# Performance work log

Hardware: AMD Instinct MI355X
Metric: run time of the kernel (lower is better)

## Reference

```python
import jax, jax.numpy as jnp
import numpy as np

N = 25000
E = 400000
IN_DIM = 512
H = 8
D = 64
ALPHA = 0.2  # leaky relu negative slope


def setup_inputs() -> dict:
    key = jax.random.key(0)
    k1, k2, k3, k4, k5 = jax.random.split(key, 5)
    inputs = jax.random.normal(k1, (N, IN_DIM), dtype=jnp.float32)
    src = jax.random.randint(k2, (E,), 0, N)
    dst = jnp.arange(E) % N  # every node has E/N inbound edges -> normalizer > 0
    # parameters (xavier-normal-ish scale)
    W = jax.random.normal(k3, (H * D, IN_DIM), dtype=jnp.float32) * (1.414 * (2.0 / (IN_DIM + H * D)) ** 0.5)
    attn_l = jax.random.normal(k4, (H, D), dtype=jnp.float32) * (1.414 * (2.0 / (D + 1)) ** 0.5)
    attn_r = jax.random.normal(k5, (H, D), dtype=jnp.float32) * (1.414 * (2.0 / (D + 1)) ** 0.5)
    return {"inputs": inputs, "W": W, "attn_l": attn_l, "attn_r": attn_r, "src": src, "dst": dst}


def reference(inputs, W, attn_l, attn_r, src, dst):
    # node projection: [N, H, D]
    ft = (inputs @ W.T).reshape(N, H, D)
    # per-node attention scalars per head: [N, H]
    a1 = jnp.einsum('nhd,hd->nh', ft, attn_l)
    a2 = jnp.einsum('nhd,hd->nh', ft, attn_r)
    # edge scores with leaky relu: [E, H]
    e = a1[src] + a2[dst]
    e = jnp.where(e > 0, e, ALPHA * e)
    # numerically stable edge softmax over incoming edges of each dst node
    emax = jax.ops.segment_max(e, dst, num_segments=N)  # [N, H]
    scores = jnp.exp(e - emax[dst])                      # [E, H]
    z = jax.ops.segment_sum(scores, dst, num_segments=N)  # [N, H]
    # weighted scatter-sum aggregation: [N, H, D]
    msg = ft[src] * scores[:, :, None]                   # [E, H, D]
    agg = jax.ops.segment_sum(msg, dst, num_segments=N)
    return agg / z[:, :, None]
```

## Files before the change

### kernel.cpp

```cpp
#include <hip/hip_runtime.h>
#include <math.h>

#define N_NODES 25000
#define E_EDGES 400000
#define IN_DIM  512
#define H_HEADS 8
#define D_HEAD  64
#define OUT_DIM 512
#define ALPHA   0.2f
#define EPN     16

typedef __attribute__((ext_vector_type(8))) short short8;
typedef __attribute__((ext_vector_type(4))) float floatx4;

__device__ __forceinline__ unsigned short f2bf(float x) {
    unsigned u = __float_as_uint(x);
    u += 0x7fffu + ((u >> 16) & 1u);
    return (unsigned short)(u >> 16);
}

#define GBM 128
#define GBN 256
#define GBK 32
#define STR 40

__global__ __launch_bounds__(512) void gemm_bf(const float* __restrict__ A,
                                               const float* __restrict__ W,
                                               const float* __restrict__ attn_l,
                                               const float* __restrict__ attn_r,
                                               unsigned short* __restrict__ ftb,
                                               float* __restrict__ a1g,
                                               float* __restrict__ a2g) {
    __shared__ unsigned short As[GBM * STR];
    __shared__ unsigned short Bs[GBN * STR];

    const int t = threadIdx.x;
    const int mbase = blockIdx.x * GBM;
    const int nbase = blockIdx.y * GBN;

    const int arow = t >> 2;
    const int akoff = (t & 3) * 8;
    const int brow = t >> 1;
    const int bkoff = (t & 1) * 16;

    const int wave = t >> 6;
    const int wm = wave & 1;
    const int wn = wave >> 1;
    const int lane = t & 63;
    const int lr = lane & 15;
    const int lq = lane >> 4;

    floatx4 acc[4][4] = {};

    const unsigned short* a_rd = As + (wm * 64 + lr) * STR + lq * 8;
    const unsigned short* b_rd = Bs + (wn * 64 + lr) * STR + lq * 8;

    const int an = mbase + arow;
    const bool a_ok = (an < N_NODES);
    const float* a_ptr0 = A + (size_t)(a_ok ? an : 0) * IN_DIM + akoff;
    const float* b_ptr0 = W + (size_t)(nbase + brow) * IN_DIM + bkoff;
    unsigned short* a_wr = As + arow * STR + akoff;
    unsigned short* b_wr = Bs + brow * STR + bkoff;

    for (int k0 = 0; k0 < IN_DIM; k0 += GBK) {
        {
            const float4* p = (const float4*)(a_ptr0 + k0);
            float4 v0 = p[0], v1 = p[1];
            if (!a_ok) { v0 = v1 = make_float4(0.f, 0.f, 0.f, 0.f); }
            short8 s0;
            s0[0]=f2bf(v0.x); s0[1]=f2bf(v0.y); s0[2]=f2bf(v0.z); s0[3]=f2bf(v0.w);
            s0[4]=f2bf(v1.x); s0[5]=f2bf(v1.y); s0[6]=f2bf(v1.z); s0[7]=f2bf(v1.w);
            *(short8*)a_wr = s0;
        }
        {
            const float4* p = (const float4*)(b_ptr0 + k0);
            float4 v0 = p[0], v1 = p[1], v2 = p[2], v3 = p[3];
            short8 s0, s1;
            s0[0]=f2bf(v0.x); s0[1]=f2bf(v0.y); s0[2]=f2bf(v0.z); s0[3]=f2bf(v0.w);
            s0[4]=f2bf(v1.x); s0[5]=f2bf(v1.y); s0[6]=f2bf(v1.z); s0[7]=f2bf(v1.w);
            s1[0]=f2bf(v2.x); s1[1]=f2bf(v2.y); s1[2]=f2bf(v2.z); s1[3]=f2bf(v2.w);
            s1[4]=f2bf(v3.x); s1[5]=f2bf(v3.y); s1[6]=f2bf(v3.z); s1[7]=f2bf(v3.w);
            *(short8*)(b_wr + 0) = s0;
            *(short8*)(b_wr + 8) = s1;
        }
        __syncthreads();

        short8 af[4], bf[4];
        #pragma unroll
        for (int i = 0; i < 4; ++i) af[i] = *(const short8*)(a_rd + i * 16 * STR);
        #pragma unroll
        for (int j = 0; j < 4; ++j) bf[j] = *(const short8*)(b_rd + j * 16 * STR);
        #pragma unroll
        for (int i = 0; i < 4; ++i)
            #pragma unroll
            for (int j = 0; j < 4; ++j)
                acc[i][j] = __builtin_amdgcn_mfma_f32_16x16x32_bf16(af[i], bf[j], acc[i][j], 0, 0, 0);
        __syncthreads();
    }

    const int h = blockIdx.y * 4 + wn;
    float al[4], ar[4];
    #pragma unroll
    for (int j = 0; j < 4; ++j) {
        al[j] = attn_l[h * D_HEAD + j * 16 + lr];
        ar[j] = attn_r[h * D_HEAD + j * 16 + lr];
    }
    #pragma unroll
    for (int i = 0; i < 4; ++i) {
        #pragma unroll
        for (int r = 0; r < 4; ++r) {
            float s1 = 0.f, s2 = 0.f;
            #pragma unroll
            for (int j = 0; j < 4; ++j) {
                s1 += acc[i][j][r] * al[j];
                s2 += acc[i][j][r] * ar[j];
            }
            #pragma unroll
            for (int off = 1; off < 16; off <<= 1) {
                s1 += __shfl_xor(s1, off, 64);
                s2 += __shfl_xor(s2, off, 64);
            }
            if (lr == 0) {
                int n = mbase + wm * 64 + i * 16 + lq * 4 + r;
                if (n < N_NODES) {
                    a1g[n * H_HEADS + h] = s1;
                    a2g[n * H_HEADS + h] = s2;
                }
            }
        }
    }

    #pragma unroll
    for (int i = 0; i < 4; ++i) {
        #pragma unroll
        for (int j = 0; j < 4; ++j) {
            const int nrow = mbase + wm * 64 + i * 16 + lq * 4;
            const int col = nbase + wn * 64 + j * 16 + lr;
            #pragma unroll
            for (int r = 0; r < 4; ++r) {
                int nn = nrow + r;
                if (nn < N_NODES)
                    ftb[(size_t)nn * OUT_DIM + col] = f2bf(acc[i][j][r]);
            }
        }
    }
}

__global__ __launch_bounds__(256) void agg_kernel(const unsigned short* __restrict__ ftb,
                                                  const float* __restrict__ a1,
                                                  const float* __restrict__ a2,
                                                  const int* __restrict__ src,
                                                  float* __restrict__ out) {
    __shared__ int   s_src[4][EPN];
    __shared__ float s_w[4][H_HEADS][EPN];
    __shared__ float s_z[4][H_HEADS];

    const int t = threadIdx.x;
    const int nd = t >> 6;
    const int r  = t & 63;
    const int v  = blockIdx.x * 4 + nd;

    if (r < EPN) s_src[nd][r] = src[v + r * N_NODES];
    __syncthreads();

    {
        const int h  = r >> 3;
        const int jp = r & 7;
        const float a2v = a2[v * H_HEADS + h];
        int s0i = s_src[nd][jp * 2], s1i = s_src[nd][jp * 2 + 1];
        float x0 = a1[s0i * H_HEADS + h] + a2v;
        float x1 = a1[s1i * H_HEADS + h] + a2v;
        float e0 = x0 > 0.f ? x0 : ALPHA * x0;
        float e1 = x1 > 0.f ? x1 : ALPHA * x1;
        float m = fmaxf(e0, e1);
        #pragma unroll
        for (int off = 1; off < 8; off <<= 1) m = fmaxf(m, __shfl_xor(m, off, 64));
        float w0 = __expf(e0 - m), w1 = __expf(e1 - m);
        s_w[nd][h][jp * 2]     = w0;
        s_w[nd][h][jp * 2 + 1] = w1;
        float z = w0 + w1;
        #pragma unroll
        for (int off = 1; off < 8; off <<= 1) z += __shfl_xor(z, off, 64);
        if (jp == 0) s_z[nd][h] = z;
    }
    __syncthreads();

    const int h   = r >> 3;
    const int oct = r & 7;
    const size_t coff = (size_t)h * D_HEAD + oct * 8;

    float acc[8] = {};
    #pragma unroll
    for (int jj = 0; jj < EPN; ++jj) {
        float wj = s_w[nd][h][jj];
        const unsigned short* p = ftb + (size_t)s_src[nd][jj] * OUT_DIM + coff;
        uint4 q = *(const uint4*)p;
        acc[0] += wj * __uint_as_float(q.x << 16);
        acc[1] += wj * __uint_as_float(q.x & 0xffff0000u);
        acc[2] += wj * __uint_as_float(q.y << 16);
        acc[3] += wj * __uint_as_float(q.y & 0xffff0000u);
        acc[4] += wj * __uint_as_float(q.z << 16);
        acc[5] += wj * __uint_as_float(q.z & 0xffff0000u);
        acc[6] += wj * __uint_as_float(q.w << 16);
        acc[7] += wj * __uint_as_float(q.w & 0xffff0000u);
    }
    float iz = 1.f / s_z[nd][h];
    float* op = out + (size_t)v * OUT_DIM + coff;
    float4 o0 = make_float4(acc[0]*iz, acc[1]*iz, acc[2]*iz, acc[3]*iz);
    float4 o1 = make_float4(acc[4]*iz, acc[5]*iz, acc[6]*iz, acc[7]*iz);
    *(float4*)(op + 0) = o0;
    *(float4*)(op + 4) = o1;
}

extern "C" void kernel_launch(void* const* d_in, const int* in_sizes, int n_in,
                              void* d_out, int out_size, void* d_ws, size_t ws_size,
                              hipStream_t stream) {
    const float* inputs = (const float*)d_in[0];
    const float* W      = (const float*)d_in[1];
    const float* attn_l = (const float*)d_in[2];
    const float* attn_r = (const float*)d_in[3];
    const int*   src    = (const int*)d_in[4];

    float* out = (float*)d_out;
    unsigned short* ftb = (unsigned short*)d_ws;
    float* a1 = (float*)(ftb + (size_t)N_NODES * OUT_DIM);
    float* a2 = a1 + (size_t)N_NODES * H_HEADS;

    dim3 gemm_grid((N_NODES + GBM - 1) / GBM, OUT_DIM / GBN);
    gemm_bf<<<gemm_grid, 512, 0, stream>>>(inputs, W, attn_l, attn_r, ftb, a1, a2);

    agg_kernel<<<N_NODES / 4, 256, 0, stream>>>(ftb, a1, a2, src, out);
}
```

Baseline: 192.3 us.

## Pre-convert inputs to bf16 and stream GEMM tiles directly into LDS

A separate conversion kernel turns the inputs and W to bf16 once. The GEMM then loads tiles with global_load_lds straight into shared memory, and each block computes a full 64x512 output tile. That way each A row is read once rather than once per column block, and per-element conversion leaves the GEMM inner loop. The GEMM output overwrites the bf16 input buffer in place to save workspace. The risks are an extra memory pass, bank conflicts from the unpadded LDS layout, and the last block reading rows past N.

```diff
diff --git a/kernel.cpp b/kernel.cpp
--- a/kernel.cpp
+++ b/kernel.cpp
@@ -19,77 +19,83 @@
     return (unsigned short)(u >> 16);
 }
 
-#define GBM 128
-#define GBN 256
+__device__ __forceinline__ void gl_lds16(const unsigned short* g, unsigned short* l) {
+    __builtin_amdgcn_global_load_lds((const __attribute__((address_space(1))) unsigned int*)g,
+                                     (__attribute__((address_space(3))) unsigned int*)l,
+                                     16, 0, 0);
+}
+
+#define A8 (N_NODES * IN_DIM / 8)
+#define W8 (OUT_DIM * IN_DIM / 8)
+
+__global__ __launch_bounds__(256) void cvt_kernel(const float* __restrict__ A,
+                                                  const float* __restrict__ W,
+                                                  unsigned short* __restrict__ Abf,
+                                                  unsigned short* __restrict__ Wbf) {
+    int idx = blockIdx.x * 256 + threadIdx.x;
+    const float* s;
+    unsigned short* d;
+    if (idx < A8) {
+        s = A + (size_t)idx * 8;
+        d = Abf + (size_t)idx * 8;
+    } else if (idx < A8 + W8) {
+        int j = idx - A8;
+        s = W + (size_t)j * 8;
+        d = Wbf + (size_t)j * 8;
+    } else {
+        return;
+    }
+    float4 v0 = ((const float4*)s)[0], v1 = ((const float4*)s)[1];
+    short8 o;
+    o[0] = f2bf(v0.x); o[1] = f2bf(v0.y); o[2] = f2bf(v0.z); o[3] = f2bf(v0.w);
+    o[4] = f2bf(v1.x); o[5] = f2bf(v1.y); o[6] = f2bf(v1.z); o[7] = f2bf(v1.w);
+    *(short8*)d = o;
+}
+
+#define GBM 64
 #define GBK 32
-#define STR 40
-
-__global__ __launch_bounds__(512) void gemm_bf(const float* __restrict__ A,
-                                               const float* __restrict__ W,
+
+__global__ __launch_bounds__(512) void gemm_bf(const unsigned short* Abf,
+                                               const unsigned short* __restrict__ Wbf,
                                                const float* __restrict__ attn_l,
                                                const float* __restrict__ attn_r,
-                                               unsigned short* __restrict__ ftb,
+                                               unsigned short* ftb,
                                                float* __restrict__ a1g,
                                                float* __restrict__ a2g) {
-    __shared__ unsigned short As[GBM * STR];
-    __shared__ unsigned short Bs[GBN * STR];
+    __shared__ unsigned short As[GBM * GBK];
+    __shared__ unsigned short Bs[OUT_DIM * GBK];
 
     const int t = threadIdx.x;
-    const int mbase = blockIdx.x * GBM;
-    const int nbase = blockIdx.y * GBN;
-
-    const int arow = t >> 2;
-    const int akoff = (t & 3) * 8;
-    const int brow = t >> 1;
-    const int bkoff = (t & 1) * 16;
-
     const int wave = t >> 6;
-    const int wm = wave & 1;
-    const int wn = wave >> 1;
     const int lane = t & 63;
     const int lr = lane & 15;
     const int lq = lane >> 4;
+    const int mb = blockIdx.x * GBM;
+
+    const int srow = lane >> 2;
+    const int schunk = (lane & 3) * 8;
+    const unsigned short* gA = Abf + (size_t)(mb + wave * 16 + srow) * IN_DIM + schunk;
+    unsigned short* lA = As + wave * 16 * GBK;
+    const unsigned short* gB = Wbf + (size_t)(wave * 64 + srow) * IN_DIM + schunk;
+    unsigned short* lB = Bs + wave * 64 * GBK;
 
     floatx4 acc[4][4] = {};
-
-    const unsigned short* a_rd = As + (wm * 64 + lr) * STR + lq * 8;
-    const unsigned short* b_rd = Bs + (wn * 64 + lr) * STR + lq * 8;
-
-    const int an = mbase + arow;
-    const bool a_ok = (an < N_NODES);
-    const float* a_ptr0 = A + (size_t)(a_ok ? an : 0) * IN_DIM + akoff;
-    const float* b_ptr0 = W + (size_t)(nbase + brow) * IN_DIM + bkoff;
-    unsigned short* a_wr = As + arow * STR + akoff;
-    unsigned short* b_wr = Bs + brow * STR + bkoff;
+    const unsigned short* a_rd = As + lr * GBK + lq * 8;
+    const unsigned short* b_rd = Bs + (wave * 64 + lr) * GBK + lq * 8;
 
     for (int k0 = 0; k0 < IN_DIM; k0 += GBK) {
-        {
-            const float4* p = (const float4*)(a_ptr0 + k0);
-            float4 v0 = p[0], v1 = p[1];
-            if (!a_ok) { v0 = v1 = make_float4(0.f, 0.f, 0.f, 0.f); }
-            short8 s0;
-            s0[0]=f2bf(v0.x); s0[1]=f2bf(v0.y); s0[2]=f2bf(v0.z); s0[3]=f2bf(v0.w);
-            s0[4]=f2bf(v1.x); s0[5]=f2bf(v1.y); s0[6]=f2bf(v1.z); s0[7]=f2bf(v1.w);
-            *(short8*)a_wr = s0;
-        }
-        {
-            const float4* p = (const float4*)(b_ptr0 + k0);
-            float4 v0 = p[0], v1 = p[1], v2 = p[2], v3 = p[3];
-            short8 s0, s1;
-            s0[0]=f2bf(v0.x); s0[1]=f2bf(v0.y); s0[2]=f2bf(v0.z); s0[3]=f2bf(v0.w);
-            s0[4]=f2bf(v1.x); s0[5]=f2bf(v1.y); s0[6]=f2bf(v1.z); s0[7]=f2bf(v1.w);
-            s1[0]=f2bf(v2.x); s1[1]=f2bf(v2.y); s1[2]=f2bf(v2.z); s1[3]=f2bf(v2.w);
-            s1[4]=f2bf(v3.x); s1[5]=f2bf(v3.y); s1[6]=f2bf(v3.z); s1[7]=f2bf(v3.w);
-            *(short8*)(b_wr + 0) = s0;
-            *(short8*)(b_wr + 8) = s1;
-        }
+        #pragma unroll
+        for (int s = 0; s < 4; ++s)
+            gl_lds16(gB + (size_t)s * 16 * IN_DIM + k0, lB + s * 16 * GBK);
+        if (wave < 4)
+            gl_lds16(gA + k0, lA);
         __syncthreads();
 
         short8 af[4], bf[4];
         #pragma unroll
-        for (int i = 0; i < 4; ++i) af[i] = *(const short8*)(a_rd + i * 16 * STR);
-        #pragma unroll
-        for (int j = 0; j < 4; ++j) bf[j] = *(const short8*)(b_rd + j * 16 * STR);
+        for (int i = 0; i < 4; ++i) af[i] = *(const short8*)(a_rd + i * 16 * GBK);
+        #pragma unroll
+        for (int j = 0; j < 4; ++j) bf[j] = *(const short8*)(b_rd + j * 16 * GBK);
         #pragma unroll
         for (int i = 0; i < 4; ++i)
             #pragma unroll
@@ -98,7 +104,7 @@
         __syncthreads();
     }
 
-    const int h = blockIdx.y * 4 + wn;
+    const int h = wave;
     float al[4], ar[4];
     #pragma unroll
     for (int j = 0; j < 4; ++j) {
@@ -121,7 +127,7 @@
                 s2 += __shfl_xor(s2, off, 64);
             }
             if (lr == 0) {
-                int n = mbase + wm * 64 + i * 16 + lq * 4 + r;
+                int n = mb + i * 16 + lq * 4 + r;
                 if (n < N_NODES) {
                     a1g[n * H_HEADS + h] = s1;
                     a2g[n * H_HEADS + h] = s2;
@@ -134,8 +140,8 @@
     for (int i = 0; i < 4; ++i) {
         #pragma unroll
         for (int j = 0; j < 4; ++j) {
-            const int nrow = mbase + wm * 64 + i * 16 + lq * 4;
-            const int col = nbase + wn * 64 + j * 16 + lr;
+            const int nrow = mb + i * 16 + lq * 4;
+            const int col = wave * 64 + j * 16 + lr;
             #pragma unroll
             for (int r = 0; r < 4; ++r) {
                 int nn = nrow + r;
@@ -206,10 +212,8 @@
     }
     float iz = 1.f / s_z[nd][h];
     float* op = out + (size_t)v * OUT_DIM + coff;
-    float4 o0 = make_float4(acc[0]*iz, acc[1]*iz, acc[2]*iz, acc[3]*iz);
-    float4 o1 = make_float4(acc[4]*iz, acc[5]*iz, acc[6]*iz, acc[7]*iz);
-    *(float4*)(op + 0) = o0;
-    *(float4*)(op + 4) = o1;
+    *(float4*)(op + 0) = make_float4(acc[0]*iz, acc[1]*iz, acc[2]*iz, acc[3]*iz);
+    *(float4*)(op + 4) = make_float4(acc[4]*iz, acc[5]*iz, acc[6]*iz, acc[7]*iz);
 }
 
 extern "C" void kernel_launch(void* const* d_in, const int* in_sizes, int n_in,
@@ -222,12 +226,15 @@
     const int*   src    = (const int*)d_in[4];
 
     float* out = (float*)d_out;
-    unsigned short* ftb = (unsigned short*)d_ws;
-    float* a1 = (float*)(ftb + (size_t)N_NODES * OUT_DIM);
+    unsigned short* buf0 = (unsigned short*)d_ws;
+    unsigned short* Wbf  = buf0 + (size_t)N_NODES * IN_DIM;
+    float* a1 = (float*)(Wbf + (size_t)OUT_DIM * IN_DIM);
     float* a2 = a1 + (size_t)N_NODES * H_HEADS;
 
-    dim3 gemm_grid((N_NODES + GBM - 1) / GBM, OUT_DIM / GBN);
-    gemm_bf<<<gemm_grid, 512, 0, stream>>>(inputs, W, attn_l, attn_r, ftb, a1, a2);
-
-    agg_kernel<<<N_NODES / 4, 256, 0, stream>>>(ftb, a1, a2, src, out);
-}
+    cvt_kernel<<<(A8 + W8 + 255) / 256, 256, 0, stream>>>(inputs, W, buf0, Wbf);
+
+    gemm_bf<<<(N_NODES + GBM - 1) / GBM, 512, 0, stream>>>(buf0, Wbf, attn_l, attn_r,
+                                                           buf0, a1, a2);
+
+    agg_kernel<<<N_NODES / 4, 256, 0, stream>>>(buf0, a1, a2, src, out);
+}
```

Measured after the change: 194.4 us. About the same (+1.1%).
